# Optimization experiments

Measured on AMD Instinct MI355X. Metric: run time of the kernel, lower is better.

Reference implementation:

```python
import jax, jax.numpy as jnp
import numpy as np

NR, NU, NS, NO = 4096, 4, 8, 8
RHO_SR, RHO_A, SIGMA, ALPHA, SIGMA_B = 0.8, 0.02, 0.084, 0.6, 1.6
BATCH, SEQ = 16, 1024


def _make_reservoir_matrix(rng):
    # Sparse random recurrent matrix: density RHO_A, rescaled to spectral radius RHO_SR.
    A = rng.uniform(-1.0, 1.0, size=(NR, NR)) * (rng.random((NR, NR)) < RHO_A)
    # Power iteration to estimate spectral radius (largest |eigenvalue|).
    v = rng.standard_normal(NR)
    for _ in range(100):
        v = A @ v
        v = v / (np.linalg.norm(v) + 1e-30)
    sr = np.linalg.norm(A @ v)
    return (A * (RHO_SR / (sr + 1e-30))).astype(np.float32)


def setup_inputs() -> dict:
    key = jax.random.key(0)
    k1, = jax.random.split(key, 1)
    rng = np.random.default_rng(0)
    inp = jax.random.normal(k1, (BATCH, SEQ, NU + NS), dtype=jnp.float32)
    r_0 = jnp.zeros((1, BATCH, NR), dtype=jnp.float32)
    A = jnp.asarray(_make_reservoir_matrix(rng))                                  # (Nr, Nr)
    B = jnp.asarray(SIGMA * rng.uniform(-1.0, 1.0, size=(NR, NU + NS)), jnp.float32)  # input matrix
    b = jnp.asarray(SIGMA_B * rng.uniform(-1.0, 1.0, size=(NR,)), jnp.float32)    # additive bias
    C_w = jnp.asarray(rng.standard_normal((NO, NR)) / np.sqrt(NR), jnp.float32)   # readout (no bias)
    return {"input": inp, "r_0": r_0, "A": A, "B": B, "b": b, "C_w": C_w}


def reference(input, r_0, A, B, b, C_w):
    # Leaky-integrator ESN recurrence over the sequence, then linear readout on the
    # final reservoir state:  r_{t+1} = (1-alpha) r_t + alpha * tanh(A r_t + B x_t + b)
    # Precompute input projections for all steps: (B, S, Nr) -> scan axis first.
    proj = jnp.einsum("bsf,nf->sbn", input, B) + b  # (S, batch, Nr)

    def step(r, p_t):
        r_new = (1.0 - ALPHA) * r + ALPHA * jnp.tanh(r @ A.T + p_t)
        return r_new, None

    r_n, _ = jax.lax.scan(step, r_0[0], proj)  # (batch, Nr)
    return r_n @ C_w.T  # (batch, No)
```

## Files before the change

kernel.cpp:

```cpp
#include <hip/hip_runtime.h>
#include <hip/hip_bf16.h>
#include <stdint.h>

#define NRR     4096
#define NBATCH  16
#define NFEAT   12
#define SEQLEN  1024
#define ALPHA_C 0.6f

typedef _Float16 f16x8 __attribute__((ext_vector_type(8)));
typedef _Float16 f16x2 __attribute__((ext_vector_type(2)));
typedef float    f32x4 __attribute__((ext_vector_type(4)));
typedef unsigned long long u64;

constexpr int WGS    = 256;
constexpr int TPB    = 512;
constexpr int WAVES  = 8;
constexpr int KCHUNK = NRR / WAVES;
constexpr int FRAGS  = KCHUNK / 32;
constexpr int SLOTE  = NBATCH * NRR;

#define SC_AGENT __HIP_MEMORY_SCOPE_AGENT

__device__ __forceinline__ unsigned ld_rlx(const unsigned* p) {
    return __hip_atomic_load(p, __ATOMIC_RELAXED, SC_AGENT);
}
__device__ __forceinline__ u64 ld_rlx64(const void* p) {
    return __hip_atomic_load((const u64*)p, __ATOMIC_RELAXED, SC_AGENT);
}
__device__ __forceinline__ void st_rlx(unsigned* p, unsigned v) {
    __hip_atomic_store(p, v, __ATOMIC_RELAXED, SC_AGENT);
}
__device__ __forceinline__ void st_rlx_f32(float* p, float v) {
    __hip_atomic_store(p, v, __ATOMIC_RELAXED, SC_AGENT);
}

__device__ __forceinline__ void gridbar(unsigned* slots, unsigned epoch,
                                        int wg, int tid, int lane, int wave,
                                        int use_inv) {
    __syncthreads();
    if (tid == 0) st_rlx(&slots[wg * 4], epoch);
    if (wave == 0) {
        const int i0 = lane * 4;
        for (;;) {
            unsigned a = ld_rlx(&slots[(i0 + 0) * 4]);
            unsigned b = ld_rlx(&slots[(i0 + 1) * 4]);
            unsigned c = ld_rlx(&slots[(i0 + 2) * 4]);
            unsigned d = ld_rlx(&slots[(i0 + 3) * 4]);
            bool ok = (a >= epoch) & (b >= epoch) & (c >= epoch) & (d >= epoch);
            if (__all(ok)) break;
        }
        if (use_inv && lane == 0)
            (void)__hip_atomic_load(&slots[wg * 4], __ATOMIC_ACQUIRE, SC_AGENT);
    }
    __syncthreads();
    asm volatile("" ::: "memory");
}

__device__ __forceinline__ float fast_tanh(float v) {
    float vc = fminf(fmaxf(v, -10.0f), 10.0f);
    float e  = __expf(2.0f * vc);
    return (e - 1.0f) * __builtin_amdgcn_rcpf(e + 1.0f);
}

__global__ __launch_bounds__(TPB, 1) void esn_persistent(
    const float* __restrict__ x,
    const float* __restrict__ r0,
    const float* __restrict__ A,
    const float* __restrict__ Bm,
    const float* __restrict__ bias,
    const float* __restrict__ Cw,
    float* __restrict__ out,
    unsigned* __restrict__ slots,
    _Float16* __restrict__ rbuf,
    float* __restrict__ rfin,
    int use_inv)
{
    const int wg    = blockIdx.x;
    const int tid   = threadIdx.x;
    const int wave  = tid >> 6;
    const int lane  = tid & 63;
    const int l15   = lane & 15;
    const int g     = lane >> 4;
    const int nbase = wg * 16;

    __shared__ float lds_red[WAVES][16][16];
    __shared__ float lds_x[2][NBATCH][NFEAT];
    __shared__ float lds_Bp[16][NFEAT];
    __shared__ float lds_bias[16];
    __shared__ float lds_out[4][128];

    uint4 afrag[FRAGS];
    {
        const float* arow = A + (size_t)(nbase + l15) * NRR + wave * KCHUNK + g * 8;
#pragma unroll
        for (int i = 0; i < FRAGS; ++i) {
            const float4* p = (const float4*)(arow + i * 32);
            float4 f0 = p[0];
            float4 f1 = p[1];
            f16x8 h;
            h[0] = (_Float16)f0.x; h[1] = (_Float16)f0.y;
            h[2] = (_Float16)f0.z; h[3] = (_Float16)f0.w;
            h[4] = (_Float16)f1.x; h[5] = (_Float16)f1.y;
            h[6] = (_Float16)f1.z; h[7] = (_Float16)f1.w;
            afrag[i] = __builtin_bit_cast(uint4, h);
        }
    }

    const int xb = tid / NFEAT;
    const int xf = tid % NFEAT;
    const size_t xofs = (size_t)xb * SEQLEN * NFEAT + xf;

    if (tid < 16 * NFEAT)
        lds_Bp[xb][xf] = Bm[(size_t)(nbase + xb) * NFEAT + xf];
    if (tid < 16)
        lds_bias[tid] = bias[nbase + tid];
    if (tid < NBATCH * NFEAT)
        lds_x[0][xb][xf] = x[xofs];

    const int ub = tid >> 4;
    const int un = tid & 15;
    float rm = 0.0f;
    if (tid < 256) {
        rm = r0[ub * NRR + nbase + un];
        float hi = __shfl_down(rm, 1);
        if (!(un & 1)) {
            f16x2 h2; h2[0] = (_Float16)rm; h2[1] = (_Float16)hi;
            st_rlx((unsigned*)(rbuf + (size_t)ub * NRR + nbase + un),
                   __builtin_bit_cast(unsigned, h2));
        }
    }

    gridbar(slots, 1u, wg, tid, lane, wave, use_inv);

    const size_t roff = (size_t)l15 * NRR + wave * KCHUNK + g * 8;

    for (int t = 0; t < SEQLEN; ++t) {
        const _Float16* rcur = rbuf + (size_t)(use_inv ? (t & 1) : t) * SLOTE;
        _Float16*       rnxt = rbuf + (size_t)(use_inv ? ((t + 1) & 1) : (t + 1)) * SLOTE;

        float xp = 0.0f;
        if (tid < NBATCH * NFEAT && t + 1 < SEQLEN)
            xp = x[xofs + (size_t)(t + 1) * NFEAT];

        f32x4 acc = {0.f, 0.f, 0.f, 0.f};
        const _Float16* rrow = rcur + roff;
#pragma unroll
        for (int i = 0; i < FRAGS; ++i) {
            uint4 u = *(const uint4*)(rrow + i * 32);
            acc = __builtin_amdgcn_mfma_f32_16x16x32_f16(
                __builtin_bit_cast(f16x8, afrag[i]),
                __builtin_bit_cast(f16x8, u), acc, 0, 0, 0);
        }
        *(f32x4*)&lds_red[wave][l15][g * 4] = acc;
        __syncthreads();

        if (tid < 256) {
            float s = 0.f;
#pragma unroll
            for (int w = 0; w < WAVES; ++w) s += lds_red[w][ub][un];
            float p = lds_bias[un];
            const float* xr = lds_x[t & 1][ub];
#pragma unroll
            for (int f = 0; f < NFEAT; ++f) p += lds_Bp[un][f] * xr[f];
            rm = (1.0f - ALPHA_C) * rm + ALPHA_C * fast_tanh(s + p);
            float hi = __shfl_down(rm, 1);
            if (!(un & 1)) {
                f16x2 h2; h2[0] = (_Float16)rm; h2[1] = (_Float16)hi;
                st_rlx((unsigned*)(rnxt + (size_t)ub * NRR + nbase + un),
                       __builtin_bit_cast(unsigned, h2));
            }
            if (t == SEQLEN - 1)
                st_rlx_f32(&rfin[(size_t)ub * NRR + nbase + un], rm);
        }
        if (tid < NBATCH * NFEAT && t + 1 < SEQLEN)
            lds_x[(t + 1) & 1][xb][xf] = xp;

        gridbar(slots, (unsigned)(t + 2), wg, tid, lane, wave, use_inv);
    }

    if (wg == 0) {
        const int oi   = tid & 127;
        const int part = tid >> 7;
        const int b = oi >> 3, o = oi & 7;
        const float* rv = rfin + (size_t)b * NRR + part * (NRR / 4);
        const float* cv = Cw   + (size_t)o * NRR + part * (NRR / 4);
        float s = 0.f;
        for (int k = 0; k < NRR / 4; k += 2) {
            u64 u = ld_rlx64(rv + k);
            float ra = __builtin_bit_cast(float, (unsigned)u);
            float rb = __builtin_bit_cast(float, (unsigned)(u >> 32));
            s += ra * cv[k] + rb * cv[k + 1];
        }
        lds_out[part][oi] = s;
        __syncthreads();
        if (tid < 128)
            out[tid] = lds_out[0][tid] + lds_out[1][tid] + lds_out[2][tid] + lds_out[3][tid];
    }
}

extern "C" void kernel_launch(void* const* d_in, const int* in_sizes, int n_in,
                              void* d_out, int out_size, void* d_ws, size_t ws_size,
                              hipStream_t stream) {
    const float* x   = (const float*)d_in[0];
    const float* r0  = (const float*)d_in[1];
    const float* A   = (const float*)d_in[2];
    const float* Bm  = (const float*)d_in[3];
    const float* bv  = (const float*)d_in[4];
    const float* Cw  = (const float*)d_in[5];
    float*       out = (float*)d_out;

    char* ws = (char*)d_ws;
    unsigned*  slots = (unsigned*)ws;
    float*     rfin  = (float*)(ws + 4096);
    _Float16*  rbuf  = (_Float16*)(ws + 4096 + 262144);

    const size_t need_stream = 4096 + 262144 + (size_t)(SEQLEN + 1) * SLOTE * 2;
    int use_inv = (ws_size >= need_stream) ? 0 : 1;

    hipMemsetAsync(ws, 0, 4096, stream);

    void* args[] = {(void*)&x, (void*)&r0, (void*)&A, (void*)&Bm, (void*)&bv, (void*)&Cw,
                    (void*)&out, (void*)&slots, (void*)&rbuf, (void*)&rfin,
                    (void*)&use_inv};
    hipError_t e = hipLaunchCooperativeKernel((const void*)esn_persistent,
                                              dim3(WGS), dim3(TPB), args, 0, stream);
    if (e != hipSuccess) {
        hipLaunchKernelGGL(esn_persistent, dim3(WGS), dim3(TPB), 0, stream,
                           x, r0, A, Bm, bv, Cw, out, slots, rbuf, rfin, use_inv);
    }
}
```

Measured before the change: 6.244 ms.

## Split batch into two independent workgroup groups with per-group barriers

The 256 workgroups are split into two groups of 128, each owning 8 batch rows and 32 reservoir rows per workgroup. The grid-wide barrier becomes a group-local barrier over 128 slots, polled with one 64-bit load per lane. Each workgroup now holds two A tiles and issues two MFMAs per fragment. Half the B-operand rows are zero-padded because each group has only 8 batch columns. A swizzled LDS reduction layout is added, and workgroup 0 waits for both groups before the readout. The aim is to cut barrier fan-in and per-step cross-workgroup traffic, at the cost of wasted MFMA lanes and more register pressure.

```diff
diff --git a/kernel.cpp b/kernel.cpp
--- a/kernel.cpp
+++ b/kernel.cpp
@@ -16,9 +16,12 @@
 constexpr int WGS    = 256;
 constexpr int TPB    = 512;
 constexpr int WAVES  = 8;
+constexpr int GWGS   = 128;
+constexpr int BPG    = 8;
+constexpr int ROWS   = 32;
 constexpr int KCHUNK = NRR / WAVES;
 constexpr int FRAGS  = KCHUNK / 32;
-constexpr int SLOTE  = NBATCH * NRR;
+constexpr int SLOTG  = BPG * NRR;
 
 #define SC_AGENT __HIP_MEMORY_SCOPE_AGENT
 
@@ -35,23 +38,20 @@
     __hip_atomic_store(p, v, __ATOMIC_RELAXED, SC_AGENT);
 }
 
-__device__ __forceinline__ void gridbar(unsigned* slots, unsigned epoch,
-                                        int wg, int tid, int lane, int wave,
-                                        int use_inv) {
+__device__ __forceinline__ void groupbar(unsigned* gslots, unsigned epoch,
+                                         int gwg, int tid, int lane, int wave,
+                                         int use_inv) {
     __syncthreads();
-    if (tid == 0) st_rlx(&slots[wg * 4], epoch);
+    if (tid == 0) st_rlx(&gslots[gwg], epoch);
     if (wave == 0) {
-        const int i0 = lane * 4;
+        const u64* sp = (const u64*)gslots;
         for (;;) {
-            unsigned a = ld_rlx(&slots[(i0 + 0) * 4]);
-            unsigned b = ld_rlx(&slots[(i0 + 1) * 4]);
-            unsigned c = ld_rlx(&slots[(i0 + 2) * 4]);
-            unsigned d = ld_rlx(&slots[(i0 + 3) * 4]);
-            bool ok = (a >= epoch) & (b >= epoch) & (c >= epoch) & (d >= epoch);
+            u64 v = ld_rlx64(&sp[lane]);
+            bool ok = ((unsigned)v >= epoch) & ((unsigned)(v >> 32) >= epoch);
             if (__all(ok)) break;
         }
         if (use_inv && lane == 0)
-            (void)__hip_atomic_load(&slots[wg * 4], __ATOMIC_ACQUIRE, SC_AGENT);
+            (void)__hip_atomic_load(&gslots[gwg], __ATOMIC_ACQUIRE, SC_AGENT);
     }
     __syncthreads();
     asm volatile("" ::: "memory");
@@ -77,22 +77,28 @@
     int use_inv)
 {
     const int wg    = blockIdx.x;
+    const int grp   = wg >> 7;
+    const int gwg   = wg & (GWGS - 1);
     const int tid   = threadIdx.x;
     const int wave  = tid >> 6;
     const int lane  = tid & 63;
     const int l15   = lane & 15;
     const int g     = lane >> 4;
-    const int nbase = wg * 16;
-
-    __shared__ float lds_red[WAVES][16][16];
-    __shared__ float lds_x[2][NBATCH][NFEAT];
-    __shared__ float lds_Bp[16][NFEAT];
-    __shared__ float lds_bias[16];
+    const int nbase = gwg * ROWS;
+
+    unsigned* gslots = slots + grp * GWGS;
+    _Float16* ring   = rbuf + (size_t)grp * (use_inv ? 2 : (SEQLEN + 1)) * SLOTG;
+
+    __shared__ float lds_red[WAVES][BPG][ROWS];
+    __shared__ float lds_x[2][BPG][NFEAT];
+    __shared__ float lds_Bp[ROWS][NFEAT];
+    __shared__ float lds_bias[ROWS];
     __shared__ float lds_out[4][128];
 
-    uint4 afrag[FRAGS];
-    {
-        const float* arow = A + (size_t)(nbase + l15) * NRR + wave * KCHUNK + g * 8;
+    uint4 afrag0[FRAGS], afrag1[FRAGS];
+#pragma unroll
+    for (int tt = 0; tt < 2; ++tt) {
+        const float* arow = A + (size_t)(nbase + tt * 16 + l15) * NRR + wave * KCHUNK + g * 8;
 #pragma unroll
         for (int i = 0; i < FRAGS; ++i) {
             const float4* p = (const float4*)(arow + i * 32);
@@ -103,62 +109,71 @@
             h[2] = (_Float16)f0.z; h[3] = (_Float16)f0.w;
             h[4] = (_Float16)f1.x; h[5] = (_Float16)f1.y;
             h[6] = (_Float16)f1.z; h[7] = (_Float16)f1.w;
-            afrag[i] = __builtin_bit_cast(uint4, h);
+            (tt == 0 ? afrag0 : afrag1)[i] = __builtin_bit_cast(uint4, h);
         }
     }
 
     const int xb = tid / NFEAT;
     const int xf = tid % NFEAT;
-    const size_t xofs = (size_t)xb * SEQLEN * NFEAT + xf;
-
-    if (tid < 16 * NFEAT)
-        lds_Bp[xb][xf] = Bm[(size_t)(nbase + xb) * NFEAT + xf];
-    if (tid < 16)
+    const size_t xofs = (size_t)(grp * BPG + xb) * SEQLEN * NFEAT + xf;
+
+    if (tid < ROWS * NFEAT)
+        lds_Bp[tid / NFEAT][tid % NFEAT] = Bm[(size_t)(nbase + tid / NFEAT) * NFEAT + tid % NFEAT];
+    if (tid < ROWS)
         lds_bias[tid] = bias[nbase + tid];
-    if (tid < NBATCH * NFEAT)
+    if (tid < BPG * NFEAT)
         lds_x[0][xb][xf] = x[xofs];
 
-    const int ub = tid >> 4;
-    const int un = tid & 15;
+    const int ub = tid >> 5;
+    const int un = tid & 31;
     float rm = 0.0f;
     if (tid < 256) {
-        rm = r0[ub * NRR + nbase + un];
+        rm = r0[(grp * BPG + ub) * NRR + nbase + un];
         float hi = __shfl_down(rm, 1);
         if (!(un & 1)) {
             f16x2 h2; h2[0] = (_Float16)rm; h2[1] = (_Float16)hi;
-            st_rlx((unsigned*)(rbuf + (size_t)ub * NRR + nbase + un),
+            st_rlx((unsigned*)(ring + (size_t)ub * NRR + nbase + un),
                    __builtin_bit_cast(unsigned, h2));
         }
     }
 
-    gridbar(slots, 1u, wg, tid, lane, wave, use_inv);
-
-    const size_t roff = (size_t)l15 * NRR + wave * KCHUNK + g * 8;
+    groupbar(gslots, 1u, gwg, tid, lane, wave, use_inv);
+
+    const size_t roff = (size_t)(l15 & 7) * NRR + wave * KCHUNK + g * 8;
+    const int    swz  = (l15 & 3) << 2;
+    const int    rsw  = ((un & 15) ^ ((ub & 3) << 2)) | (un & 16);
 
     for (int t = 0; t < SEQLEN; ++t) {
-        const _Float16* rcur = rbuf + (size_t)(use_inv ? (t & 1) : t) * SLOTE;
-        _Float16*       rnxt = rbuf + (size_t)(use_inv ? ((t + 1) & 1) : (t + 1)) * SLOTE;
+        const _Float16* rcur = ring + (size_t)(use_inv ? (t & 1) : t) * SLOTG;
+        _Float16*       rnxt = ring + (size_t)(use_inv ? ((t + 1) & 1) : (t + 1)) * SLOTG;
 
         float xp = 0.0f;
-        if (tid < NBATCH * NFEAT && t + 1 < SEQLEN)
+        if (tid < BPG * NFEAT && t + 1 < SEQLEN)
             xp = x[xofs + (size_t)(t + 1) * NFEAT];
 
-        f32x4 acc = {0.f, 0.f, 0.f, 0.f};
+        f32x4 acc0 = {0.f, 0.f, 0.f, 0.f};
+        f32x4 acc1 = {0.f, 0.f, 0.f, 0.f};
         const _Float16* rrow = rcur + roff;
 #pragma unroll
         for (int i = 0; i < FRAGS; ++i) {
-            uint4 u = *(const uint4*)(rrow + i * 32);
-            acc = __builtin_amdgcn_mfma_f32_16x16x32_f16(
-                __builtin_bit_cast(f16x8, afrag[i]),
-                __builtin_bit_cast(f16x8, u), acc, 0, 0, 0);
-        }
-        *(f32x4*)&lds_red[wave][l15][g * 4] = acc;
+            uint4 u = {0u, 0u, 0u, 0u};
+            if (l15 < 8) u = *(const uint4*)(rrow + i * 32);
+            f16x8 rv = __builtin_bit_cast(f16x8, u);
+            acc0 = __builtin_amdgcn_mfma_f32_16x16x32_f16(
+                __builtin_bit_cast(f16x8, afrag0[i]), rv, acc0, 0, 0, 0);
+            acc1 = __builtin_amdgcn_mfma_f32_16x16x32_f16(
+                __builtin_bit_cast(f16x8, afrag1[i]), rv, acc1, 0, 0, 0);
+        }
+        if (l15 < 8) {
+            *(f32x4*)&lds_red[wave][l15][(g * 4) ^ swz]      = acc0;
+            *(f32x4*)&lds_red[wave][l15][16 + ((g * 4) ^ swz)] = acc1;
+        }
         __syncthreads();
 
         if (tid < 256) {
             float s = 0.f;
 #pragma unroll
-            for (int w = 0; w < WAVES; ++w) s += lds_red[w][ub][un];
+            for (int w = 0; w < WAVES; ++w) s += lds_red[w][ub][rsw];
             float p = lds_bias[un];
             const float* xr = lds_x[t & 1][ub];
 #pragma unroll
@@ -171,15 +186,27 @@
                        __builtin_bit_cast(unsigned, h2));
             }
             if (t == SEQLEN - 1)
-                st_rlx_f32(&rfin[(size_t)ub * NRR + nbase + un], rm);
-        }
-        if (tid < NBATCH * NFEAT && t + 1 < SEQLEN)
+                st_rlx_f32(&rfin[(size_t)(grp * BPG + ub) * NRR + nbase + un], rm);
+        }
+        if (tid < BPG * NFEAT && t + 1 < SEQLEN)
             lds_x[(t + 1) & 1][xb][xf] = xp;
 
-        gridbar(slots, (unsigned)(t + 2), wg, tid, lane, wave, use_inv);
+        groupbar(gslots, (unsigned)(t + 2), gwg, tid, lane, wave, use_inv);
     }
 
     if (wg == 0) {
+        if (wave == 0) {
+            const u64* sp = (const u64*)slots;
+            const unsigned fin = SEQLEN + 1u;
+            for (;;) {
+                u64 a = ld_rlx64(&sp[lane]);
+                u64 b = ld_rlx64(&sp[64 + lane]);
+                bool ok = ((unsigned)a >= fin) & ((unsigned)(a >> 32) >= fin) &
+                          ((unsigned)b >= fin) & ((unsigned)(b >> 32) >= fin);
+                if (__all(ok)) break;
+            }
+        }
+        __syncthreads();
         const int oi   = tid & 127;
         const int part = tid >> 7;
         const int b = oi >> 3, o = oi & 7;
@@ -215,7 +242,7 @@
     float*     rfin  = (float*)(ws + 4096);
     _Float16*  rbuf  = (_Float16*)(ws + 4096 + 262144);
 
-    const size_t need_stream = 4096 + 262144 + (size_t)(SEQLEN + 1) * SLOTE * 2;
+    const size_t need_stream = 4096 + 262144 + 2 * (size_t)(SEQLEN + 1) * SLOTG * 2;
     int use_inv = (ws_size >= need_stream) ? 0 : 1;
 
     hipMemsetAsync(ws, 0, 4096, stream);
```

Result: slower. 8.488 ms (+35.9%).
